# Kernel optimization log

Hardware: AMD Instinct MI355X
Metric: run time of the kernel (lower is better)

## Reference

```python
import jax, jax.numpy as jnp
import numpy as np
import math

N, NF, D, HEADS, LEVELS, POINTS = 1, 2, 256, 8, 4, 4
SPATIAL = np.array([[100, 100], [50, 50], [25, 25], [13, 13]], dtype=np.int32)
LEN_IN = int((SPATIAL[:, 0] * SPATIAL[:, 1]).sum())  # 13294
LEN_Q = LEN_IN


def _grid_init_bias():
    # faithful to MSDeformAttn._reset_parameters
    thetas = np.arange(HEADS, dtype=np.float32) * (2.0 * math.pi / HEADS)
    grid = np.stack([np.cos(thetas), np.sin(thetas)], -1)
    grid = grid / np.abs(grid).max(-1, keepdims=True)
    grid = np.tile(grid.reshape(HEADS, 1, 1, 2), (1, LEVELS, POINTS, 1))
    for i in range(POINTS):
        grid[:, :, i, :] *= i + 1
    return grid.reshape(-1).astype(np.float32)  # [HEADS*LEVELS*POINTS*2]


def setup_inputs() -> dict:
    key = jax.random.key(0)
    ks = jax.random.split(key, 8)
    lsi = np.concatenate([[0], np.cumsum(SPATIAL[:, 0] * SPATIAL[:, 1])[:-1]]).astype(np.int32)
    s = 1.0 / math.sqrt(D)
    return {
        "query": jax.random.normal(ks[0], (N, NF, LEN_Q, D), jnp.float32),
        "reference_points": jax.random.uniform(ks[1], (N, LEN_Q, LEVELS, 2), jnp.float32),
        "input_flatten": jax.random.normal(ks[2], (N, NF, LEN_IN, D), jnp.float32),
        "input_spatial_shapes": jnp.asarray(SPATIAL),
        "input_level_start_index": jnp.asarray(lsi),
        "Wv": jax.random.normal(ks[3], (D, D), jnp.float32) * s,
        "bv": jnp.zeros((D,), jnp.float32),
        "Woff": jax.random.normal(ks[4], (D, HEADS * LEVELS * POINTS * 2), jnp.float32) * 0.01,
        "boff": jnp.asarray(_grid_init_bias()),
        "Wattn": jax.random.normal(ks[5], (D, HEADS * LEVELS * POINTS), jnp.float32) * 0.02,
        "battn": jnp.zeros((HEADS * LEVELS * POINTS,), jnp.float32),
        "Wout": jax.random.normal(ks[6], (D, D), jnp.float32) * s,
        "bout": jnp.zeros((D,), jnp.float32),
    }


def ms_deform_attn_core(value, spatial_shapes, level_start_index, loc, attn):
    """value: [B, Lin, H, Dh]; loc: [B, Lq, H, L, P, 2] in [0,1]; attn: [B, Lq, H, L, P].
    Bilinear sampling matches F.grid_sample(align_corners=False, padding_mode='zeros')
    applied to grid = 2*loc - 1, i.e. pixel coord = loc*size - 0.5."""
    B, Lin, Hn, Dh = value.shape
    Lq, L, P = loc.shape[1], loc.shape[3], loc.shape[4]
    val_t = value.transpose(0, 2, 1, 3)  # [B, H, Lin, Dh]
    out = jnp.zeros((B, Lq, Hn, Dh), value.dtype)
    for l in range(L):
        Hl = spatial_shapes[l, 0]
        Wl = spatial_shapes[l, 1]
        start = level_start_index[l]
        x = loc[:, :, :, l, :, 0] * Wl - 0.5  # [B, Lq, H, P]
        y = loc[:, :, :, l, :, 1] * Hl - 0.5
        x0 = jnp.floor(x)
        y0 = jnp.floor(y)
        lx, ly = x - x0, y - y0
        x0i = x0.astype(jnp.int32)
        y0i = y0.astype(jnp.int32)
        sampled = jnp.zeros((B, Lq, Hn, P, Dh), value.dtype)
        corners = [(0, 0, (1 - lx) * (1 - ly)), (0, 1, lx * (1 - ly)),
                   (1, 0, (1 - lx) * ly), (1, 1, lx * ly)]
        for dy, dx, w in corners:
            xi = x0i + dx
            yi = y0i + dy
            valid = (xi >= 0) & (xi < Wl) & (yi >= 0) & (yi < Hl)
            idx = start + jnp.clip(yi, 0, Hl - 1) * Wl + jnp.clip(xi, 0, Wl - 1)
            idx_t = idx.transpose(0, 2, 1, 3).reshape(B, Hn, Lq * P)  # [B, H, Lq*P]
            v = jnp.take_along_axis(val_t, idx_t[:, :, :, None], axis=2)  # [B, H, Lq*P, Dh]
            v = v.reshape(B, Hn, Lq, P, Dh).transpose(0, 2, 1, 3, 4)  # [B, Lq, H, P, Dh]
            sampled = sampled + jnp.where(valid, w, 0.0)[..., None] * v
        out = out + jnp.einsum('blhp,blhpd->blhd', attn[:, :, :, l, :], sampled)
    return out.reshape(B, Lq, Hn * Dh)


def reference(query, reference_points, input_flatten, input_spatial_shapes,
              input_level_start_index, Wv, bv, Woff, boff, Wattn, battn, Wout, bout):
    n, nf, Lq, d = query.shape
    Lin = input_flatten.shape[2]
    Dh = d // HEADS
    value = (input_flatten @ Wv + bv).reshape(n * nf, Lin, HEADS, Dh)
    off = (query @ Woff + boff).reshape(n, nf, Lq, HEADS, LEVELS, POINTS, 2)
    aw = (query @ Wattn + battn).reshape(n, nf, Lq, HEADS, LEVELS * POINTS)
    aw = jax.nn.softmax(aw, axis=-1).reshape(n, nf, Lq, HEADS, LEVELS, POINTS)
    # offset normalizer: [W, H] per level
    norm = jnp.stack([input_spatial_shapes[:, 1], input_spatial_shapes[:, 0]], -1).astype(query.dtype)
    # reference_points: [n, Lq, L, 2] -> broadcast with offsets [n, nf, Lq, H, L, P, 2]
    loc = reference_points[:, None, :, None, :, None, :] + off / norm[None, None, None, None, :, None, :]
    loc = loc.reshape(n * nf, Lq, HEADS, LEVELS, POINTS, 2)
    aw = aw.reshape(n * nf, Lq, HEADS, LEVELS, POINTS)
    out = ms_deform_attn_core(value, input_spatial_shapes, input_level_start_index, loc, aw)
    out = out.reshape(n, nf, Lq, d)
    return out @ Wout + bout
```

## Files before the change

### kernel.cpp

```cpp
#include <hip/hip_runtime.h>
#include <math.h>

#define LEN_Q 13294
#define NFRAMES 2
#define MTOT (LEN_Q * NFRAMES)
#define HEADS 8
#define LEVELS 4
#define POINTS 4

typedef __attribute__((ext_vector_type(8))) short short8;
typedef __attribute__((ext_vector_type(4))) float f32x4;
typedef __attribute__((ext_vector_type(4))) int i32x4;
typedef __attribute__((ext_vector_type(2))) unsigned int uint2v;
typedef __attribute__((ext_vector_type(4))) unsigned short ushort4v;

__device__ __forceinline__ unsigned short f2bf(float x) {
    unsigned u = __builtin_bit_cast(unsigned, x);
    unsigned r = (u + 0x7fffu + ((u >> 16) & 1u)) >> 16;
    return (unsigned short)r;
}
__device__ __forceinline__ float bf2f(unsigned short b) {
    return __builtin_bit_cast(float, (unsigned)b << 16);
}

#define LSTR 40

__global__ __launch_bounds__(256) void prep_weights(
    const float* __restrict__ Wv,  const float* __restrict__ Woff,
    const float* __restrict__ Wat, const float* __restrict__ Wout,
    unsigned short* __restrict__ wvT,
    unsigned short* __restrict__ woaT,
    unsigned short* __restrict__ woutT)
{
    const int b = blockIdx.x;
    const int k = threadIdx.x;
    const float* src; unsigned short* dst; int N; int n;
    if (b < 256)      { src = Wv;   dst = wvT;          N = 256; n = b; }
    else if (b < 512) { src = Woff; dst = woaT;         N = 256; n = b - 256; }
    else if (b < 640) { src = Wat;  dst = woaT + 65536; N = 128; n = b - 512; }
    else              { src = Wout; dst = woutT;        N = 256; n = b - 640; }
    dst[(size_t)n * 256 + k] = f2bf(src[(size_t)k * N + n]);
}

__global__ __launch_bounds__(256, 3) void gemm_fused(
    const float* __restrict__ Aval,
    const float* __restrict__ Aq,
    const unsigned short* __restrict__ BTv,
    const unsigned short* __restrict__ BToa,
    const float* __restrict__ bv,
    const float* __restrict__ boff,
    const float* __restrict__ battn,
    unsigned short* __restrict__ v16,
    unsigned short* __restrict__ off16,
    unsigned short* __restrict__ at16,
    int M, int K)
{
    __shared__ unsigned short As[128 * LSTR];
    __shared__ unsigned short Bs[128 * LSTR];

    const int t = threadIdx.x;
    const int w = t >> 6;
    const int L = t & 63;
    const int m0 = blockIdx.y * 128;
    const bool isVal = (blockIdx.x < 2);
    const int nTile = isVal ? blockIdx.x : blockIdx.x - 2;
    const float* Af = isVal ? Aval : Aq;
    const unsigned short* BTb = (isVal ? BTv : BToa) + (size_t)nTile * 128 * K;

    const int sr = t >> 1;
    const int sc = (t & 1) * 16;
    int arow = m0 + sr; if (arow > M - 1) arow = M - 1;
    const float* Ag = Af + (size_t)arow * K + sc;
    const unsigned short* Bg = BTb + (size_t)sr * K + sc;
    unsigned short* AsW = &As[sr * LSTR + sc];
    unsigned short* BsW = &Bs[sr * LSTR + sc];

    const int mq = (w & 1) * 64;
    const int nq = (w >> 1) * 64;
    const int lr = L & 15;
    const int kq = (L >> 4) * 8;

    f32x4 acc[4][4];
    #pragma unroll
    for (int i = 0; i < 4; ++i)
        #pragma unroll
        for (int j = 0; j < 4; ++j) acc[i][j] = (f32x4){0.f, 0.f, 0.f, 0.f};

    f32x4 a0 = *(const f32x4*)(Ag);
    f32x4 a1 = *(const f32x4*)(Ag + 4);
    f32x4 a2 = *(const f32x4*)(Ag + 8);
    f32x4 a3 = *(const f32x4*)(Ag + 12);
    short8 b0 = *(const short8*)(Bg);
    short8 b1 = *(const short8*)(Bg + 8);

    for (int k0 = 0; k0 < K; k0 += 32) {
        short8 p0, p1;
        p0[0]=(short)f2bf(a0.x); p0[1]=(short)f2bf(a0.y); p0[2]=(short)f2bf(a0.z); p0[3]=(short)f2bf(a0.w);
        p0[4]=(short)f2bf(a1.x); p0[5]=(short)f2bf(a1.y); p0[6]=(short)f2bf(a1.z); p0[7]=(short)f2bf(a1.w);
        p1[0]=(short)f2bf(a2.x); p1[1]=(short)f2bf(a2.y); p1[2]=(short)f2bf(a2.z); p1[3]=(short)f2bf(a2.w);
        p1[4]=(short)f2bf(a3.x); p1[5]=(short)f2bf(a3.y); p1[6]=(short)f2bf(a3.z); p1[7]=(short)f2bf(a3.w);
        __syncthreads();
        *(short8*)(AsW) = p0;
        *(short8*)(AsW + 8) = p1;
        *(short8*)(BsW) = b0;
        *(short8*)(BsW + 8) = b1;
        __syncthreads();

        if (k0 + 32 < K) {
            a0 = *(const f32x4*)(Ag + k0 + 32);
            a1 = *(const f32x4*)(Ag + k0 + 36);
            a2 = *(const f32x4*)(Ag + k0 + 40);
            a3 = *(const f32x4*)(Ag + k0 + 44);
            b0 = *(const short8*)(Bg + k0 + 32);
            b1 = *(const short8*)(Bg + k0 + 40);
        }

        short8 af[4], bf[4];
        #pragma unroll
        for (int i = 0; i < 4; ++i)
            af[i] = *(const short8*)&As[(mq + i * 16 + lr) * LSTR + kq];
        #pragma unroll
        for (int j = 0; j < 4; ++j)
            bf[j] = *(const short8*)&Bs[(nq + j * 16 + lr) * LSTR + kq];
        #pragma unroll
        for (int i = 0; i < 4; ++i)
            #pragma unroll
            for (int j = 0; j < 4; ++j)
                acc[i][j] = __builtin_amdgcn_mfma_f32_16x16x32_bf16(af[i], bf[j], acc[i][j], 0, 0, 0);
    }

    const int rr = (L >> 4) * 4;
    #pragma unroll
    for (int i = 0; i < 4; ++i) {
        #pragma unroll
        for (int r = 0; r < 4; ++r) {
            int m = m0 + mq + i * 16 + rr + r;
            if (m < M) {
                #pragma unroll
                for (int j = 0; j < 4; ++j) {
                    int colg = nTile * 128 + nq + j * 16 + lr;
                    float v = acc[i][j][r];
                    if (isVal) {
                        v16[(size_t)m * 256 + colg] = f2bf(v + bv[colg]);
                    } else if (colg < 256) {
                        off16[(size_t)m * 256 + colg] = f2bf(v + boff[colg]);
                    } else {
                        at16[(size_t)m * 128 + (colg - 256)] = f2bf(v + battn[colg - 256]);
                    }
                }
            }
        }
    }
}

__global__ __launch_bounds__(256, 3) void gemm_out(
    const unsigned short* __restrict__ A,
    const unsigned short* __restrict__ BT,
    const float* __restrict__ bias,
    float* __restrict__ C,
    int M, int K)
{
    __shared__ unsigned short As[128 * LSTR];
    __shared__ unsigned short Bs[128 * LSTR];

    const int t = threadIdx.x;
    const int w = t >> 6;
    const int L = t & 63;
    const int m0 = blockIdx.y * 128;
    const int n0 = blockIdx.x * 128;

    const int sr = t >> 1;
    const int sc = (t & 1) * 16;
    int arow = m0 + sr; if (arow > M - 1) arow = M - 1;
    const unsigned short* Ag = A + (size_t)arow * K + sc;
    const unsigned short* Bg = BT + (size_t)(n0 + sr) * K + sc;
    unsigned short* AsW = &As[sr * LSTR + sc];
    unsigned short* BsW = &Bs[sr * LSTR + sc];

    const int mq = (w & 1) * 64;
    const int nq = (w >> 1) * 64;
    const int lr = L & 15;
    const int kq = (L >> 4) * 8;

    f32x4 acc[4][4];
    #pragma unroll
    for (int i = 0; i < 4; ++i)
        #pragma unroll
        for (int j = 0; j < 4; ++j) acc[i][j] = (f32x4){0.f, 0.f, 0.f, 0.f};

    short8 a0 = *(const short8*)(Ag);
    short8 a1 = *(const short8*)(Ag + 8);
    short8 b0 = *(const short8*)(Bg);
    short8 b1 = *(const short8*)(Bg + 8);

    for (int k0 = 0; k0 < K; k0 += 32) {
        __syncthreads();
        *(short8*)(AsW) = a0;
        *(short8*)(AsW + 8) = a1;
        *(short8*)(BsW) = b0;
        *(short8*)(BsW + 8) = b1;
        __syncthreads();

        if (k0 + 32 < K) {
            a0 = *(const short8*)(Ag + k0 + 32);
            a1 = *(const short8*)(Ag + k0 + 40);
            b0 = *(const short8*)(Bg + k0 + 32);
            b1 = *(const short8*)(Bg + k0 + 40);
        }

        short8 af[4], bf[4];
        #pragma unroll
        for (int i = 0; i < 4; ++i)
            af[i] = *(const short8*)&As[(mq + i * 16 + lr) * LSTR + kq];
        #pragma unroll
        for (int j = 0; j < 4; ++j)
            bf[j] = *(const short8*)&Bs[(nq + j * 16 + lr) * LSTR + kq];
        #pragma unroll
        for (int i = 0; i < 4; ++i)
            #pragma unroll
            for (int j = 0; j < 4; ++j)
                acc[i][j] = __builtin_amdgcn_mfma_f32_16x16x32_bf16(af[i], bf[j], acc[i][j], 0, 0, 0);
    }

    const int rr = (L >> 4) * 4;
    #pragma unroll
    for (int i = 0; i < 4; ++i) {
        #pragma unroll
        for (int r = 0; r < 4; ++r) {
            int m = m0 + mq + i * 16 + rr + r;
            if (m < M) {
                #pragma unroll
                for (int j = 0; j < 4; ++j) {
                    int n = n0 + nq + j * 16 + lr;
                    C[(size_t)m * 256 + n] = acc[i][j][r] + bias[n];
                }
            }
        }
    }
}

__global__ __launch_bounds__(256) void sample9(
    const unsigned short* __restrict__ value,
    const unsigned short* __restrict__ off,
    const unsigned short* __restrict__ attn,
    const float* __restrict__ refpts,
    const int*   __restrict__ spatial,
    const int*   __restrict__ lsi,
    unsigned short* __restrict__ samp)
{
    const int b = blockIdx.x;
    const int h = b & 7;
    const int chunk = b >> 3;
    const int t = threadIdx.x;
    const int rl = t >> 3;
    const int j = t & 7;

    int row = chunk * 32 + rl;
    const bool valid = row < MTOT;
    if (row > MTOT - 1) row = MTOT - 1;
    const int frame = row >= LEN_Q ? 1 : 0;
    const int q = row - frame * LEN_Q;

    __shared__ float w_s[32][68];
    __shared__ int   idx_s[32][68];

    uint2v ov = *(const uint2v*)(off + (size_t)row * 256 + h * 32 + j * 4);
    unsigned av = *(const unsigned*)(attn + (size_t)row * 128 + h * 16 + j * 2);
    float t0 = bf2f((unsigned short)(av & 0xffffu));
    float t1 = bf2f((unsigned short)(av >> 16));

    float m = fmaxf(t0, t1);
    #pragma unroll
    for (int d = 1; d < 8; d <<= 1) m = fmaxf(m, __shfl_xor(m, d));
    float e0 = __expf(t0 - m);
    float e1 = __expf(t1 - m);
    float s = e0 + e1;
    #pragma unroll
    for (int d = 1; d < 8; d <<= 1) s += __shfl_xor(s, d);
    float inv = 1.f / s;
    float wt01[2] = { e0 * inv, e1 * inv };

    {
        const int l = j >> 1;
        const int Hl = spatial[l * 2], Wl = spatial[l * 2 + 1];
        const int start = lsi[l];
        const int voff0 = frame * (LEN_Q * 512) + h * 64;
        const float rx = refpts[((size_t)q * LEVELS + l) * 2];
        const float ry = refpts[((size_t)q * LEVELS + l) * 2 + 1];
        #pragma unroll
        for (int i = 0; i < 2; ++i) {
            const int lp = 2 * j + i;
            unsigned sel = (i == 0) ? ov.x : ov.y;
            float ox = bf2f((unsigned short)(sel & 0xffffu));
            float oy = bf2f((unsigned short)(sel >> 16));
            float locx = rx + ox * __builtin_amdgcn_rcpf((float)Wl);
            float locy = ry + oy * __builtin_amdgcn_rcpf((float)Hl);
            float wt = wt01[i];
            float x = locx * (float)Wl - 0.5f;
            float y = locy * (float)Hl - 0.5f;
            float x0f = floorf(x), y0f = floorf(y);
            float lx = x - x0f, ly = y - y0f;
            int x0 = (int)x0f, y0 = (int)y0f;
            int x1 = x0 + 1, y1 = y0 + 1;
            int vx0 = (x0 >= 0) & (x0 < Wl);
            int vx1 = (x1 >= 0) & (x1 < Wl);
            int vy0 = (y0 >= 0) & (y0 < Hl);
            int vy1 = (y1 >= 0) & (y1 < Hl);
            int x0c = min(max(x0, 0), Wl - 1);
            int x1c = min(max(x1, 0), Wl - 1);
            int y0c = min(max(y0, 0), Hl - 1);
            int y1c = min(max(y1, 0), Hl - 1);
            i32x4 iv;
            iv.x = voff0 + (start + y0c * Wl + x0c) * 512;
            iv.y = voff0 + (start + y0c * Wl + x1c) * 512;
            iv.z = voff0 + (start + y1c * Wl + x0c) * 512;
            iv.w = voff0 + (start + y1c * Wl + x1c) * 512;
            f32x4 wv;
            wv.x = (vy0 & vx0) ? wt * (1.f - lx) * (1.f - ly) : 0.f;
            wv.y = (vy0 & vx1) ? wt * lx * (1.f - ly) : 0.f;
            wv.z = (vy1 & vx0) ? wt * (1.f - lx) * ly : 0.f;
            wv.w = (vy1 & vx1) ? wt * lx * ly : 0.f;
            *(i32x4*)&idx_s[rl][lp * 4] = iv;
            *(f32x4*)&w_s[rl][lp * 4] = wv;
        }
    }
    __syncthreads();

    const char* vb = (const char*)value;
    const unsigned lane8 = (unsigned)(j * 8);

    f32x4  wreg[2][2];
    uint2v vbuf[2][8];
    auto fetch = [&](int buf, int g) {
        wreg[buf][0] = *(const f32x4*)&w_s[rl][(2 * g) * 4];
        wreg[buf][1] = *(const f32x4*)&w_s[rl][(2 * g + 1) * 4];
        i32x4 i0 = *(const i32x4*)&idx_s[rl][(2 * g) * 4];
        i32x4 i1 = *(const i32x4*)&idx_s[rl][(2 * g + 1) * 4];
        vbuf[buf][0] = *(const uint2v*)(vb + (unsigned)(i0.x) + lane8);
        vbuf[buf][1] = *(const uint2v*)(vb + (unsigned)(i0.y) + lane8);
        vbuf[buf][2] = *(const uint2v*)(vb + (unsigned)(i0.z) + lane8);
        vbuf[buf][3] = *(const uint2v*)(vb + (unsigned)(i0.w) + lane8);
        vbuf[buf][4] = *(const uint2v*)(vb + (unsigned)(i1.x) + lane8);
        vbuf[buf][5] = *(const uint2v*)(vb + (unsigned)(i1.y) + lane8);
        vbuf[buf][6] = *(const uint2v*)(vb + (unsigned)(i1.z) + lane8);
        vbuf[buf][7] = *(const uint2v*)(vb + (unsigned)(i1.w) + lane8);
    };

    float a0 = 0.f, a1 = 0.f, a2 = 0.f, a3 = 0.f;
    fetch(0, 0);
    #pragma unroll
    for (int g = 0; g < 8; ++g) {
        const int cur = g & 1;
        if (g < 7) fetch(cur ^ 1, g + 1);
        #pragma unroll
        for (int p = 0; p < 2; ++p) {
            f32x4 wv = wreg[cur][p];
            #pragma unroll
            for (int c = 0; c < 4; ++c) {
                float wc = wv[c];
                uint2v v = vbuf[cur][p * 4 + c];
                a0 = fmaf(wc, __builtin_bit_cast(float, v.x << 16), a0);
                a1 = fmaf(wc, __builtin_bit_cast(float, v.x & 0xffff0000u), a1);
                a2 = fmaf(wc, __builtin_bit_cast(float, v.y << 16), a2);
                a3 = fmaf(wc, __builtin_bit_cast(float, v.y & 0xffff0000u), a3);
            }
        }
    }
    if (valid) {
        ushort4v o;
        o.x = f2bf(a0); o.y = f2bf(a1); o.z = f2bf(a2); o.w = f2bf(a3);
        *(ushort4v*)(samp + (size_t)row * 256 + h * 32 + j * 4) = o;
    }
}

extern "C" void kernel_launch(void* const* d_in, const int* in_sizes, int n_in,
                              void* d_out, int out_size, void* d_ws, size_t ws_size,
                              hipStream_t stream)
{
    const float* query   = (const float*)d_in[0];
    const float* refpts  = (const float*)d_in[1];
    const float* inflat  = (const float*)d_in[2];
    const int*   spatial = (const int*)d_in[3];
    const int*   lsi     = (const int*)d_in[4];
    const float* Wv      = (const float*)d_in[5];
    const float* bv      = (const float*)d_in[6];
    const float* Woff    = (const float*)d_in[7];
    const float* boff    = (const float*)d_in[8];
    const float* Wattn   = (const float*)d_in[9];
    const float* battn   = (const float*)d_in[10];
    const float* Wout    = (const float*)d_in[11];
    const float* bout    = (const float*)d_in[12];

    unsigned short* ws = (unsigned short*)d_ws;
    const size_t MR = (size_t)MTOT * 256;
    unsigned short* v16    = ws;
    unsigned short* off16  = v16 + MR;
    unsigned short* at16   = off16 + MR;
    unsigned short* samp16 = at16 + (size_t)MTOT * 128;
    unsigned short* wvT    = samp16 + MR;
    unsigned short* woaT   = wvT + 65536;
    unsigned short* woutT  = woaT + 98304;

    dim3 blk256(256);
    const int mBlocks = (MTOT + 127) / 128;

    hipLaunchKernelGGL(prep_weights, dim3(896), blk256, 0, stream,
                       Wv, Woff, Wattn, Wout, wvT, woaT, woutT);

    hipLaunchKernelGGL(gemm_fused, dim3(5, mBlocks), blk256, 0, stream,
                       inflat, query, wvT, woaT, bv, boff, battn,
                       v16, off16, at16, MTOT, 256);

    hipLaunchKernelGGL(sample9, dim3(6648), blk256, 0, stream,
                       v16, off16, at16, refpts, spatial, lsi, samp16);

    hipLaunchKernelGGL(gemm_out, dim3(2, mBlocks), blk256, 0, stream,
                       samp16, woutT, bout, (float*)d_out, MTOT, 256);
}
```

Before: 228.2 us.

## Store value in head-major layout with x-neighbor duplication for paired bilinear loads

The value projection now writes a head-major layout in which each pixel slot also holds the next pixel's features. One 16-byte load then fetches both horizontal bilinear neighbors, so each sample point needs two wide loads instead of four narrow ones. The sampler clamps each point's base corner to the interior and folds out-of-bounds handling into the corner weights. Lanes split the work by x-neighbor and combine partial sums with a shuffle. The cost is roughly doubled value storage and scattered duplicate writes in the GEMM epilogue, plus extra shuffles and idle lanes at store time.

```diff
diff --git a/kernel.cpp b/kernel.cpp
--- a/kernel.cpp
+++ b/kernel.cpp
@@ -2,6 +2,7 @@
 #include <math.h>
 
 #define LEN_Q 13294
+#define LEN_IN 13294
 #define NFRAMES 2
 #define MTOT (LEN_Q * NFRAMES)
 #define HEADS 8
@@ -12,6 +13,7 @@
 typedef __attribute__((ext_vector_type(4))) float f32x4;
 typedef __attribute__((ext_vector_type(4))) int i32x4;
 typedef __attribute__((ext_vector_type(2))) unsigned int uint2v;
+typedef __attribute__((ext_vector_type(4))) unsigned int uint4v;
 typedef __attribute__((ext_vector_type(4))) unsigned short ushort4v;
 
 __device__ __forceinline__ unsigned short f2bf(float x) {
@@ -21,6 +23,12 @@
 }
 __device__ __forceinline__ float bf2f(unsigned short b) {
     return __builtin_bit_cast(float, (unsigned)b << 16);
+}
+__device__ __forceinline__ float bfl(unsigned u) {
+    return __builtin_bit_cast(float, u << 16);
+}
+__device__ __forceinline__ float bfh(unsigned u) {
+    return __builtin_bit_cast(float, u & 0xffff0000u);
 }
 
 #define LSTR 40
@@ -50,7 +58,7 @@
     const float* __restrict__ bv,
     const float* __restrict__ boff,
     const float* __restrict__ battn,
-    unsigned short* __restrict__ v16,
+    unsigned short* __restrict__ vdup,
     unsigned short* __restrict__ off16,
     unsigned short* __restrict__ at16,
     int M, int K)
@@ -141,7 +149,13 @@
                     int colg = nTile * 128 + nq + j * 16 + lr;
                     float v = acc[i][j][r];
                     if (isVal) {
-                        v16[(size_t)m * 256 + colg] = f2bf(v + bv[colg]);
+                        int hh = colg >> 5, d = colg & 31;
+                        int fr = (m >= LEN_Q) ? 1 : 0;
+                        int e = m - fr * LEN_Q;
+                        size_t ebase = ((size_t)(fr * 8 + hh) * (LEN_IN + 1) + e) * 64;
+                        unsigned short bvv = f2bf(v + bv[colg]);
+                        vdup[ebase + d] = bvv;
+                        if (e > 0) vdup[ebase - 64 + 32 + d] = bvv;
                     } else if (colg < 256) {
                         off16[(size_t)m * 256 + colg] = f2bf(v + boff[colg]);
                     } else {
@@ -239,8 +253,8 @@
     }
 }
 
-__global__ __launch_bounds__(256) void sample9(
-    const unsigned short* __restrict__ value,
+__global__ __launch_bounds__(256) void sample10(
+    const unsigned short* __restrict__ vdup,
     const unsigned short* __restrict__ off,
     const unsigned short* __restrict__ attn,
     const float* __restrict__ refpts,
@@ -262,7 +276,7 @@
     const int q = row - frame * LEN_Q;
 
     __shared__ float w_s[32][68];
-    __shared__ int   idx_s[32][68];
+    __shared__ int   b_s[32][20];
 
     uint2v ov = *(const uint2v*)(off + (size_t)row * 256 + h * 32 + j * 4);
     unsigned av = *(const unsigned*)(attn + (size_t)row * 128 + h * 16 + j * 2);
@@ -284,7 +298,7 @@
         const int l = j >> 1;
         const int Hl = spatial[l * 2], Wl = spatial[l * 2 + 1];
         const int start = lsi[l];
-        const int voff0 = frame * (LEN_Q * 512) + h * 64;
+        const int slab = (frame * 8 + h) * (LEN_IN + 1);
         const float rx = refpts[((size_t)q * LEVELS + l) * 2];
         const float ry = refpts[((size_t)q * LEVELS + l) * 2 + 1];
         #pragma unroll
@@ -301,52 +315,48 @@
             float x0f = floorf(x), y0f = floorf(y);
             float lx = x - x0f, ly = y - y0f;
             int x0 = (int)x0f, y0 = (int)y0f;
-            int x1 = x0 + 1, y1 = y0 + 1;
-            int vx0 = (x0 >= 0) & (x0 < Wl);
-            int vx1 = (x1 >= 0) & (x1 < Wl);
-            int vy0 = (y0 >= 0) & (y0 < Hl);
-            int vy1 = (y1 >= 0) & (y1 < Hl);
-            int x0c = min(max(x0, 0), Wl - 1);
-            int x1c = min(max(x1, 0), Wl - 1);
-            int y0c = min(max(y0, 0), Hl - 1);
-            int y1c = min(max(y1, 0), Hl - 1);
-            i32x4 iv;
-            iv.x = voff0 + (start + y0c * Wl + x0c) * 512;
-            iv.y = voff0 + (start + y0c * Wl + x1c) * 512;
-            iv.z = voff0 + (start + y1c * Wl + x0c) * 512;
-            iv.w = voff0 + (start + y1c * Wl + x1c) * 512;
+            int xbase = min(max(x0, 0), Wl - 2);
+            int ybase = min(max(y0, 0), Hl - 2);
+            float wxe0 = (x0 == xbase) ? (1.f - lx) : ((x0 == -1) ? lx : 0.f);
+            float wxe1 = (x0 == xbase) ? lx : ((x0 == Wl - 1) ? (1.f - lx) : 0.f);
+            float wye0 = (y0 == ybase) ? (1.f - ly) : ((y0 == -1) ? ly : 0.f);
+            float wye1 = (y0 == ybase) ? ly : ((y0 == Hl - 1) ? (1.f - ly) : 0.f);
+            b_s[rl][lp] = (slab + start + ybase * Wl + xbase) * 128;
             f32x4 wv;
-            wv.x = (vy0 & vx0) ? wt * (1.f - lx) * (1.f - ly) : 0.f;
-            wv.y = (vy0 & vx1) ? wt * lx * (1.f - ly) : 0.f;
-            wv.z = (vy1 & vx0) ? wt * (1.f - lx) * ly : 0.f;
-            wv.w = (vy1 & vx1) ? wt * lx * ly : 0.f;
-            *(i32x4*)&idx_s[rl][lp * 4] = iv;
+            wv.x = wt * wxe0 * wye0;
+            wv.y = wt * wxe1 * wye0;
+            wv.z = wt * wxe0 * wye1;
+            wv.w = wt * wxe1 * wye1;
             *(f32x4*)&w_s[rl][lp * 4] = wv;
         }
     }
     __syncthreads();
 
-    const char* vb = (const char*)value;
-    const unsigned lane8 = (unsigned)(j * 8);
+    const char* vb = (const char*)vdup;
+    const unsigned lane16 = (unsigned)(j * 16);
+    const int hi = (j >> 2) & 1;
+    int ystr[4];
+    #pragma unroll
+    for (int l2 = 0; l2 < 4; ++l2) ystr[l2] = spatial[l2 * 2 + 1] * 128;
 
     f32x4  wreg[2][2];
-    uint2v vbuf[2][8];
+    uint4v vbuf[2][4];
     auto fetch = [&](int buf, int g) {
         wreg[buf][0] = *(const f32x4*)&w_s[rl][(2 * g) * 4];
         wreg[buf][1] = *(const f32x4*)&w_s[rl][(2 * g + 1) * 4];
-        i32x4 i0 = *(const i32x4*)&idx_s[rl][(2 * g) * 4];
-        i32x4 i1 = *(const i32x4*)&idx_s[rl][(2 * g + 1) * 4];
-        vbuf[buf][0] = *(const uint2v*)(vb + (unsigned)(i0.x) + lane8);
-        vbuf[buf][1] = *(const uint2v*)(vb + (unsigned)(i0.y) + lane8);
-        vbuf[buf][2] = *(const uint2v*)(vb + (unsigned)(i0.z) + lane8);
-        vbuf[buf][3] = *(const uint2v*)(vb + (unsigned)(i0.w) + lane8);
-        vbuf[buf][4] = *(const uint2v*)(vb + (unsigned)(i1.x) + lane8);
-        vbuf[buf][5] = *(const uint2v*)(vb + (unsigned)(i1.y) + lane8);
-        vbuf[buf][6] = *(const uint2v*)(vb + (unsigned)(i1.z) + lane8);
-        vbuf[buf][7] = *(const uint2v*)(vb + (unsigned)(i1.w) + lane8);
+        int b0 = b_s[rl][2 * g];
+        int b1 = b_s[rl][2 * g + 1];
+        int ys = ystr[g >> 1];
+        vbuf[buf][0] = *(const uint4v*)(vb + (unsigned)b0 + lane16);
+        vbuf[buf][1] = *(const uint4v*)(vb + (unsigned)(b0 + ys) + lane16);
+        vbuf[buf][2] = *(const uint4v*)(vb + (unsigned)b1 + lane16);
+        vbuf[buf][3] = *(const uint4v*)(vb + (unsigned)(b1 + ys) + lane16);
     };
 
-    float a0 = 0.f, a1 = 0.f, a2 = 0.f, a3 = 0.f;
+    float a[8];
+    #pragma unroll
+    for (int k = 0; k < 8; ++k) a[k] = 0.f;
+
     fetch(0, 0);
     #pragma unroll
     for (int g = 0; g < 8; ++g) {
@@ -354,22 +364,31 @@
         if (g < 7) fetch(cur ^ 1, g + 1);
         #pragma unroll
         for (int p = 0; p < 2; ++p) {
-            f32x4 wv = wreg[cur][p];
+            f32x4 w4 = wreg[cur][p];
+            float wy0 = hi ? w4.y : w4.x;
+            float wy1 = hi ? w4.w : w4.z;
+            uint4v v0 = vbuf[cur][p * 2];
+            uint4v v1 = vbuf[cur][p * 2 + 1];
             #pragma unroll
-            for (int c = 0; c < 4; ++c) {
-                float wc = wv[c];
-                uint2v v = vbuf[cur][p * 4 + c];
-                a0 = fmaf(wc, __builtin_bit_cast(float, v.x << 16), a0);
-                a1 = fmaf(wc, __builtin_bit_cast(float, v.x & 0xffff0000u), a1);
-                a2 = fmaf(wc, __builtin_bit_cast(float, v.y << 16), a2);
-                a3 = fmaf(wc, __builtin_bit_cast(float, v.y & 0xffff0000u), a3);
+            for (int k = 0; k < 4; ++k) {
+                unsigned u0 = v0[k], u1 = v1[k];
+                a[2 * k]     = fmaf(wy0, bfl(u0), a[2 * k]);
+                a[2 * k + 1] = fmaf(wy0, bfh(u0), a[2 * k + 1]);
+                a[2 * k]     = fmaf(wy1, bfl(u1), a[2 * k]);
+                a[2 * k + 1] = fmaf(wy1, bfh(u1), a[2 * k + 1]);
             }
         }
     }
-    if (valid) {
-        ushort4v o;
-        o.x = f2bf(a0); o.y = f2bf(a1); o.z = f2bf(a2); o.w = f2bf(a3);
-        *(ushort4v*)(samp + (size_t)row * 256 + h * 32 + j * 4) = o;
+
+    #pragma unroll
+    for (int k = 0; k < 8; ++k) a[k] += __shfl_xor(a[k], 4);
+
+    if (valid && hi == 0) {
+        uint4v o;
+        #pragma unroll
+        for (int k = 0; k < 4; ++k)
+            o[k] = (unsigned)f2bf(a[2 * k]) | ((unsigned)f2bf(a[2 * k + 1]) << 16);
+        *(uint4v*)(samp + (size_t)row * 256 + h * 32 + (j & 3) * 8) = o;
     }
 }
 
@@ -393,8 +412,9 @@
 
     unsigned short* ws = (unsigned short*)d_ws;
     const size_t MR = (size_t)MTOT * 256;
-    unsigned short* v16    = ws;
-    unsigned short* off16  = v16 + MR;
+    const size_t VDUP = (size_t)16 * (LEN_IN + 1) * 64;
+    unsigned short* vdup   = ws;
+    unsigned short* off16  = vdup + VDUP;
     unsigned short* at16   = off16 + MR;
     unsigned short* samp16 = at16 + (size_t)MTOT * 128;
     unsigned short* wvT    = samp16 + MR;
@@ -409,10 +429,10 @@
 
     hipLaunchKernelGGL(gemm_fused, dim3(5, mBlocks), blk256, 0, stream,
                        inflat, query, wvT, woaT, bv, boff, battn,
-                       v16, off16, at16, MTOT, 256);
-
-    hipLaunchKernelGGL(sample9, dim3(6648), blk256, 0, stream,
-                       v16, off16, at16, refpts, spatial, lsi, samp16);
+                       vdup, off16, at16, MTOT, 256);
+
+    hipLaunchKernelGGL(sample10, dim3(6648), blk256, 0, stream,
+                       vdup, off16, at16, refpts, spatial, lsi, samp16);
 
     hipLaunchKernelGGL(gemm_out, dim3(2, mBlocks), blk256, 0, stream,
                        samp16, woutT, bout, (float*)d_out, MTOT, 256);
```

Result: faster. 207.2 us (-9.2%).
